# Kernel optimization log

Measured on AMD Instinct MI355X. Metric: run time of the kernel, lower is better.

Reference implementation:

```python
import jax, jax.numpy as jnp
import numpy as np

N = 500000   # num_nodes
B = 512      # batch_size
D = 128      # node_dim
G = 128      # global_dim
MC = 64      # max_cubes
M = 24       # max_moves_per_cube
H = 128      # MLP hidden
NEG = -1000000000.0


def setup_inputs() -> dict:
    key = jax.random.key(0)
    ks = jax.random.split(key, 8)
    node_features = jax.random.normal(ks[0], (N, D), jnp.float32)
    global_features = jax.random.normal(ks[1], (B, G), jnp.float32)
    cube_mask = jax.random.randint(ks[2], (N,), 0, 2) == 1
    batch = jnp.sort(jax.random.randint(ks[3], (N,), 0, B))
    move_mask = jax.random.randint(ks[4], (B, MC, M), 0, 2) == 1
    W1 = jax.random.normal(ks[5], (D + G, H), jnp.float32) * 0.05
    b1 = jnp.zeros((H,), jnp.float32)
    W2 = jax.random.normal(ks[6], (H, M), jnp.float32) * 0.05
    b2 = jnp.zeros((M,), jnp.float32)
    return {"node_features": node_features, "global_features": global_features,
            "W1": W1, "b1": b1, "W2": W2, "b2": b2,
            "cube_mask": cube_mask, "batch": batch, "move_mask": move_mask}


def reference(node_features, global_features, W1, b1, W2, b2, cube_mask, batch, move_mask):
    bsz = global_features.shape[0]
    max_cubes, moves = move_mask.shape[1], move_mask.shape[2]
    batch = batch.astype(jnp.int32)

    # gather global features per node, concat, small MLP (scores computed for all
    # nodes; only cube-node rows are ever scattered, matching the original math)
    combined = jnp.concatenate([node_features, global_features[batch]], axis=-1)  # [N, D+G]
    h = jax.nn.relu(combined @ W1 + b1)                                           # [N, H]
    scores = h @ W2 + b2                                                          # [N, M]

    # per-batch cumulative cube count (batch is sorted): cube_idx_in_batch
    mask_i = cube_mask.astype(jnp.int32)
    cum = jnp.cumsum(mask_i)                                   # inclusive prefix count of cubes
    counts = jax.ops.segment_sum(mask_i, batch, num_segments=bsz)
    offsets = jnp.concatenate([jnp.zeros((1,), jnp.int32),
                               jnp.cumsum(counts)[:-1].astype(jnp.int32)])
    cube_idx = cum - 1 - offsets[batch]                        # index of cube within its graph

    valid = cube_mask & (cube_idx < max_cubes)
    ib = jnp.where(valid, batch, bsz)      # out-of-range rows -> dropped
    ic = jnp.where(valid, cube_idx, 0)

    logits = jnp.full((bsz, max_cubes, moves), NEG, dtype=scores.dtype)
    logits = logits.at[ib, ic].set(scores, mode="drop")        # unique (ib, ic) per valid node

    logits_flat = logits.reshape(bsz, -1)
    logits_flat = jnp.where(move_mask.reshape(bsz, -1), logits_flat, NEG)
    return logits_flat
```

## Files before the change

### kernel.cpp

```cpp
#include <hip/hip_runtime.h>

typedef short bf16x8 __attribute__((ext_vector_type(8)));
typedef float f32x4 __attribute__((ext_vector_type(4)));

#define NEGV -1000000000.0f

__device__ __forceinline__ unsigned short f2bf(float f) {
    unsigned int u = __float_as_uint(f);
    u += 0x7FFFu + ((u >> 16) & 1u);
    return (unsigned short)(u >> 16);
}

__global__ void prep_kernel(const float* __restrict__ W1, const float* __restrict__ W2,
                            const int* __restrict__ batch, int N, int B,
                            int* __restrict__ batch_start,
                            unsigned short* __restrict__ w1t, unsigned short* __restrict__ w2t) {
    int idx = blockIdx.x * 256 + threadIdx.x;
    if (idx < N) {
        int bcur = batch[idx];
        if (idx == 0) {
            for (int bb = 0; bb <= bcur; ++bb) batch_start[bb] = 0;
        } else {
            int bprev = batch[idx - 1];
            for (int bb = bprev + 1; bb <= bcur; ++bb) batch_start[bb] = idx;
        }
        if (idx == N - 1) {
            for (int bb = bcur + 1; bb <= B; ++bb) batch_start[bb] = N;
        }
    }
    if (idx < 128 * 256) {
        int col = idx >> 8, k = idx & 255;
        w1t[col * 256 + k] = f2bf(W1[k * 128 + col]);
    }
    if (idx < 32 * 128) {
        int col = idx >> 7, k = idx & 127;
        w2t[col * 128 + k] = (col < 24) ? f2bf(W2[k * 24 + col]) : (unsigned short)0;
    }
}

__global__ void __launch_bounds__(256, 2)
fused_kernel(const float* __restrict__ nf, const float* __restrict__ gf,
             const unsigned short* __restrict__ w1t, const unsigned short* __restrict__ w2t,
             const float* __restrict__ b1, const float* __restrict__ b2,
             const int* __restrict__ cube_mask, const int* __restrict__ batch_start,
             const int* __restrict__ move_mask, float* __restrict__ out) {
    __shared__ __align__(16) unsigned short ldsA[64][72];
    __shared__ __align__(16) unsigned short ldsB[128][72];
    __shared__ __align__(16) unsigned short ldsH[64][136];
    __shared__ __align__(16) unsigned short ldsW2[32][136];
    __shared__ int lds_node[64];
    __shared__ int wt[4];

    int t = threadIdx.x;
    int blk = blockIdx.x;
    int lane = t & 63, w = t >> 6;

    if (t < 64) lds_node[t] = -1;
    {
        int col = t >> 3;
        int k0 = (t & 7) * 16;
        const unsigned short* src = w2t + col * 128 + k0;
        *(bf16x8*)&ldsW2[col][k0]     = *(const bf16x8*)(src);
        *(bf16x8*)&ldsW2[col][k0 + 8] = *(const bf16x8*)(src + 8);
    }
    int segs = batch_start[blk], sege = batch_start[blk + 1];
    __syncthreads();

    int found = 0;
    for (int pos = segs; pos < sege && found < 64; pos += 256) {
        int i = pos + t;
        int m = (i < sege) ? cube_mask[i] : 0;
        unsigned long long bal = __ballot(m != 0);
        int below = __popcll(bal & ((1ULL << lane) - 1ULL));
        if (lane == 0) wt[w] = __popcll(bal);
        __syncthreads();
        int waveOfs = 0, total = 0;
#pragma unroll
        for (int j = 0; j < 4; ++j) { int c = wt[j]; if (j < w) waveOfs += c; total += c; }
        int rank = found + waveOfs + below;
        if (m && rank < 64) lds_node[rank] = i;
        found += total;
        __syncthreads();
    }
    __syncthreads();

    int wm = w >> 1, wn = w & 1;
    f32x4 acc[2][4];
#pragma unroll
    for (int i = 0; i < 2; ++i)
#pragma unroll
        for (int j = 0; j < 4; ++j) acc[i][j] = (f32x4){0.f, 0.f, 0.f, 0.f};

    int r = t >> 2;
    int q = t & 3;
    int n = lds_node[r];
    int nrow = (n >= 0) ? n : 0;

    float4 fA[4];
    bf16x8 fB[4];
    int bcol = t >> 1;
    int bh0 = (t & 1) * 32;

#define LOAD_A(c) do { \
        const float* srcA = ((c) < 2) ? nf + (size_t)nrow * 128 + (c) * 64 + q * 16 \
                                      : gf + (size_t)blk * 128 + ((c) - 2) * 64 + q * 16; \
        fA[0] = *(const float4*)(srcA);      fA[1] = *(const float4*)(srcA + 4); \
        fA[2] = *(const float4*)(srcA + 8);  fA[3] = *(const float4*)(srcA + 12); \
    } while (0)
#define LOAD_B(c) do { \
        const unsigned short* srcB = w1t + bcol * 256 + (c) * 64 + bh0; \
        fB[0] = *(const bf16x8*)(srcB);      fB[1] = *(const bf16x8*)(srcB + 8); \
        fB[2] = *(const bf16x8*)(srcB + 16); fB[3] = *(const bf16x8*)(srcB + 24); \
    } while (0)

    LOAD_A(0); LOAD_B(0);
#pragma unroll
    for (int c = 0; c < 4; ++c) {
        {
            unsigned short tmp[16];
#pragma unroll
            for (int i = 0; i < 4; ++i) {
                tmp[i * 4 + 0] = f2bf(fA[i].x); tmp[i * 4 + 1] = f2bf(fA[i].y);
                tmp[i * 4 + 2] = f2bf(fA[i].z); tmp[i * 4 + 3] = f2bf(fA[i].w);
            }
            *(bf16x8*)&ldsA[r][q * 16]     = *(bf16x8*)&tmp[0];
            *(bf16x8*)&ldsA[r][q * 16 + 8] = *(bf16x8*)&tmp[8];
            *(bf16x8*)&ldsB[bcol][bh0]      = fB[0];
            *(bf16x8*)&ldsB[bcol][bh0 + 8]  = fB[1];
            *(bf16x8*)&ldsB[bcol][bh0 + 16] = fB[2];
            *(bf16x8*)&ldsB[bcol][bh0 + 24] = fB[3];
        }
        __syncthreads();
        if (c < 3) { LOAD_A(c + 1); LOAD_B(c + 1); }
#pragma unroll
        for (int ks = 0; ks < 2; ++ks) {
            int ko = ks * 32 + (lane >> 4) * 8;
            bf16x8 af[2], bfr[4];
#pragma unroll
            for (int mt = 0; mt < 2; ++mt)
                af[mt] = *(const bf16x8*)&ldsA[wm * 32 + mt * 16 + (lane & 15)][ko];
#pragma unroll
            for (int nt = 0; nt < 4; ++nt)
                bfr[nt] = *(const bf16x8*)&ldsB[wn * 64 + nt * 16 + (lane & 15)][ko];
#pragma unroll
            for (int mt = 0; mt < 2; ++mt)
#pragma unroll
                for (int nt = 0; nt < 4; ++nt)
                    acc[mt][nt] = __builtin_amdgcn_mfma_f32_16x16x32_bf16(
                        af[mt], bfr[nt], acc[mt][nt], 0, 0, 0);
        }
        __syncthreads();
    }
#undef LOAD_A
#undef LOAD_B

#pragma unroll
    for (int nt = 0; nt < 4; ++nt) {
        int col = wn * 64 + nt * 16 + (lane & 15);
        float bias = b1[col];
#pragma unroll
        for (int mt = 0; mt < 2; ++mt) {
            int row0 = wm * 32 + mt * 16 + (lane >> 4) * 4;
#pragma unroll
            for (int rr = 0; rr < 4; ++rr) {
                float v = acc[mt][nt][rr] + bias;
                v = v > 0.f ? v : 0.f;
                ldsH[row0 + rr][col] = f2bf(v);
            }
        }
    }
    __syncthreads();

    f32x4 acc2[2];
    acc2[0] = (f32x4){0.f, 0.f, 0.f, 0.f};
    acc2[1] = (f32x4){0.f, 0.f, 0.f, 0.f};
#pragma unroll
    for (int ks = 0; ks < 4; ++ks) {
        int ko = ks * 32 + (lane >> 4) * 8;
        bf16x8 a2 = *(const bf16x8*)&ldsH[w * 16 + (lane & 15)][ko];
#pragma unroll
        for (int ct = 0; ct < 2; ++ct) {
            bf16x8 bw = *(const bf16x8*)&ldsW2[ct * 16 + (lane & 15)][ko];
            acc2[ct] = __builtin_amdgcn_mfma_f32_16x16x32_bf16(a2, bw, acc2[ct], 0, 0, 0);
        }
    }

#pragma unroll
    for (int ct = 0; ct < 2; ++ct) {
        int m = ct * 16 + (lane & 15);
        if (m >= 24) continue;
        float bias = b2[m];
#pragma unroll
        for (int rr = 0; rr < 4; ++rr) {
            int row = w * 16 + (lane >> 4) * 4 + rr;
            int slot = blk * 64 + row;
            size_t oidx = (size_t)slot * 24 + m;
            float v = acc2[ct][rr] + bias;
            bool keep = (lds_node[row] >= 0) && (move_mask[oidx] != 0);
            out[oidx] = keep ? v : NEGV;
        }
    }
}

extern "C" void kernel_launch(void* const* d_in, const int* in_sizes, int n_in,
                              void* d_out, int out_size, void* d_ws, size_t ws_size,
                              hipStream_t stream) {
    const float* nf = (const float*)d_in[0];
    const float* gf = (const float*)d_in[1];
    const float* W1 = (const float*)d_in[2];
    const float* b1 = (const float*)d_in[3];
    const float* W2 = (const float*)d_in[4];
    const float* b2 = (const float*)d_in[5];
    const int* cube_mask = (const int*)d_in[6];
    const int* batch     = (const int*)d_in[7];
    const int* move_mask = (const int*)d_in[8];
    float* out = (float*)d_out;

    int N = in_sizes[6];
    int B = in_sizes[1] / 128;

    char* ws = (char*)d_ws;
    int* batch_start = (int*)(ws);
    unsigned short* w1t = (unsigned short*)(ws + 4096);
    unsigned short* w2t = (unsigned short*)(ws + 69632);

    int NB = (N + 255) / 256;
    prep_kernel<<<NB, 256, 0, stream>>>(W1, W2, batch, N, B, batch_start, w1t, w2t);
    fused_kernel<<<B, 256, 0, stream>>>(nf, gf, w1t, w2t, b1, b2,
                                        cube_mask, batch_start, move_mask, out);
    (void)n_in; (void)out_size; (void)ws_size;
}
```

Measured before the change: 20.15 us.

## Hoist weight, bias and mask loads early, prefetch node rows, alias LDS

The fused kernel now issues the first W1 tile, the biases and the move_mask values before the cube-compaction scan, so their latency hides behind the scan. Both node-feature chunks are loaded right after compaction instead of chunk by chunk. The H buffer is aliased onto the A/B staging LDS, and launch bounds go from 2 to 3 blocks per SM to allow more occupancy. The cost is higher register pressure from the extra prefetched values, which may cause spills under the tighter launch bound.

Result: faster. 17.86 us, median of 3 (-11.4%).

```diff
diff --git a/kernel.cpp b/kernel.cpp
--- a/kernel.cpp
+++ b/kernel.cpp
@@ -38,24 +38,28 @@
     }
 }
 
-__global__ void __launch_bounds__(256, 2)
+__global__ void __launch_bounds__(256, 3)
 fused_kernel(const float* __restrict__ nf, const float* __restrict__ gf,
              const unsigned short* __restrict__ w1t, const unsigned short* __restrict__ w2t,
              const float* __restrict__ b1, const float* __restrict__ b2,
              const int* __restrict__ cube_mask, const int* __restrict__ batch_start,
              const int* __restrict__ move_mask, float* __restrict__ out) {
-    __shared__ __align__(16) unsigned short ldsA[64][72];
-    __shared__ __align__(16) unsigned short ldsB[128][72];
-    __shared__ __align__(16) unsigned short ldsH[64][136];
+    __shared__ __align__(16) char smemAB[(64 * 72 + 128 * 72) * 2];
     __shared__ __align__(16) unsigned short ldsW2[32][136];
     __shared__ int lds_node[64];
     __shared__ int wt[4];
+    unsigned short (*ldsA)[72]  = (unsigned short (*)[72])smemAB;
+    unsigned short (*ldsB)[72]  = (unsigned short (*)[72])(smemAB + 64 * 72 * 2);
+    unsigned short (*ldsH)[136] = (unsigned short (*)[136])smemAB;
 
     int t = threadIdx.x;
     int blk = blockIdx.x;
     int lane = t & 63, w = t >> 6;
 
+    int segs = batch_start[blk], sege = batch_start[blk + 1];
+
     if (t < 64) lds_node[t] = -1;
+
     {
         int col = t >> 3;
         int k0 = (t & 7) * 16;
@@ -63,7 +67,35 @@
         *(bf16x8*)&ldsW2[col][k0]     = *(const bf16x8*)(src);
         *(bf16x8*)&ldsW2[col][k0 + 8] = *(const bf16x8*)(src + 8);
     }
-    int segs = batch_start[blk], sege = batch_start[blk + 1];
+    int bcol = t >> 1, bh0 = (t & 1) * 32;
+    bf16x8 fB[4];
+    {
+        const unsigned short* srcB = w1t + bcol * 256 + bh0;
+        fB[0] = *(const bf16x8*)(srcB);      fB[1] = *(const bf16x8*)(srcB + 8);
+        fB[2] = *(const bf16x8*)(srcB + 16); fB[3] = *(const bf16x8*)(srcB + 24);
+    }
+    int wm = w >> 1, wn = w & 1;
+    float b1v[4];
+#pragma unroll
+    for (int nt = 0; nt < 4; ++nt) b1v[nt] = b1[wn * 64 + nt * 16 + (lane & 15)];
+    float b2v[2];
+    int mmv[8];
+#pragma unroll
+    for (int ct = 0; ct < 2; ++ct) {
+        int m = ct * 16 + (lane & 15);
+        if (m < 24) {
+            b2v[ct] = b2[m];
+#pragma unroll
+            for (int rr = 0; rr < 4; ++rr) {
+                int row = w * 16 + (lane >> 4) * 4 + rr;
+                mmv[ct * 4 + rr] = move_mask[(size_t)(blk * 64 + row) * 24 + m];
+            }
+        } else {
+            b2v[ct] = 0.f;
+#pragma unroll
+            for (int rr = 0; rr < 4; ++rr) mmv[ct * 4 + rr] = 0;
+        }
+    }
     __syncthreads();
 
     int found = 0;
@@ -82,47 +114,40 @@
         found += total;
         __syncthreads();
     }
-    __syncthreads();
-
-    int wm = w >> 1, wn = w & 1;
-    f32x4 acc[2][4];
-#pragma unroll
-    for (int i = 0; i < 2; ++i)
-#pragma unroll
-        for (int j = 0; j < 4; ++j) acc[i][j] = (f32x4){0.f, 0.f, 0.f, 0.f};
 
     int r = t >> 2;
     int q = t & 3;
     int n = lds_node[r];
     int nrow = (n >= 0) ? n : 0;
 
+    const float* srcN = nf + (size_t)nrow * 128 + q * 16;
+    float4 fN[8];
+#pragma unroll
+    for (int i = 0; i < 4; ++i) {
+        fN[i]     = *(const float4*)(srcN + i * 4);
+        fN[4 + i] = *(const float4*)(srcN + 64 + i * 4);
+    }
+
+    f32x4 acc[2][4];
+#pragma unroll
+    for (int i = 0; i < 2; ++i)
+#pragma unroll
+        for (int j = 0; j < 4; ++j) acc[i][j] = (f32x4){0.f, 0.f, 0.f, 0.f};
+
     float4 fA[4];
-    bf16x8 fB[4];
-    int bcol = t >> 1;
-    int bh0 = (t & 1) * 32;
-
-#define LOAD_A(c) do { \
-        const float* srcA = ((c) < 2) ? nf + (size_t)nrow * 128 + (c) * 64 + q * 16 \
-                                      : gf + (size_t)blk * 128 + ((c) - 2) * 64 + q * 16; \
-        fA[0] = *(const float4*)(srcA);      fA[1] = *(const float4*)(srcA + 4); \
-        fA[2] = *(const float4*)(srcA + 8);  fA[3] = *(const float4*)(srcA + 12); \
-    } while (0)
-#define LOAD_B(c) do { \
-        const unsigned short* srcB = w1t + bcol * 256 + (c) * 64 + bh0; \
-        fB[0] = *(const bf16x8*)(srcB);      fB[1] = *(const bf16x8*)(srcB + 8); \
-        fB[2] = *(const bf16x8*)(srcB + 16); fB[3] = *(const bf16x8*)(srcB + 24); \
-    } while (0)
-
-    LOAD_A(0); LOAD_B(0);
+
 #pragma unroll
     for (int c = 0; c < 4; ++c) {
         {
+            float4 s0 = (c == 0) ? fN[0] : (c == 1) ? fN[4] : fA[0];
+            float4 s1 = (c == 0) ? fN[1] : (c == 1) ? fN[5] : fA[1];
+            float4 s2 = (c == 0) ? fN[2] : (c == 1) ? fN[6] : fA[2];
+            float4 s3 = (c == 0) ? fN[3] : (c == 1) ? fN[7] : fA[3];
             unsigned short tmp[16];
-#pragma unroll
-            for (int i = 0; i < 4; ++i) {
-                tmp[i * 4 + 0] = f2bf(fA[i].x); tmp[i * 4 + 1] = f2bf(fA[i].y);
-                tmp[i * 4 + 2] = f2bf(fA[i].z); tmp[i * 4 + 3] = f2bf(fA[i].w);
-            }
+            tmp[0]  = f2bf(s0.x); tmp[1]  = f2bf(s0.y); tmp[2]  = f2bf(s0.z); tmp[3]  = f2bf(s0.w);
+            tmp[4]  = f2bf(s1.x); tmp[5]  = f2bf(s1.y); tmp[6]  = f2bf(s1.z); tmp[7]  = f2bf(s1.w);
+            tmp[8]  = f2bf(s2.x); tmp[9]  = f2bf(s2.y); tmp[10] = f2bf(s2.z); tmp[11] = f2bf(s2.w);
+            tmp[12] = f2bf(s3.x); tmp[13] = f2bf(s3.y); tmp[14] = f2bf(s3.z); tmp[15] = f2bf(s3.w);
             *(bf16x8*)&ldsA[r][q * 16]     = *(bf16x8*)&tmp[0];
             *(bf16x8*)&ldsA[r][q * 16 + 8] = *(bf16x8*)&tmp[8];
             *(bf16x8*)&ldsB[bcol][bh0]      = fB[0];
@@ -131,7 +156,16 @@
             *(bf16x8*)&ldsB[bcol][bh0 + 24] = fB[3];
         }
         __syncthreads();
-        if (c < 3) { LOAD_A(c + 1); LOAD_B(c + 1); }
+        if (c < 3) {
+            const unsigned short* srcB = w1t + bcol * 256 + (c + 1) * 64 + bh0;
+            fB[0] = *(const bf16x8*)(srcB);      fB[1] = *(const bf16x8*)(srcB + 8);
+            fB[2] = *(const bf16x8*)(srcB + 16); fB[3] = *(const bf16x8*)(srcB + 24);
+        }
+        if (c == 1 || c == 2) {
+            const float* srcG = gf + (size_t)blk * 128 + (c - 1) * 64 + q * 16;
+            fA[0] = *(const float4*)(srcG);     fA[1] = *(const float4*)(srcG + 4);
+            fA[2] = *(const float4*)(srcG + 8); fA[3] = *(const float4*)(srcG + 12);
+        }
 #pragma unroll
         for (int ks = 0; ks < 2; ++ks) {
             int ko = ks * 32 + (lane >> 4) * 8;
@@ -151,13 +185,11 @@
         }
         __syncthreads();
     }
-#undef LOAD_A
-#undef LOAD_B
 
 #pragma unroll
     for (int nt = 0; nt < 4; ++nt) {
         int col = wn * 64 + nt * 16 + (lane & 15);
-        float bias = b1[col];
+        float bias = b1v[nt];
 #pragma unroll
         for (int mt = 0; mt < 2; ++mt) {
             int row0 = wm * 32 + mt * 16 + (lane >> 4) * 4;
@@ -189,14 +221,12 @@
     for (int ct = 0; ct < 2; ++ct) {
         int m = ct * 16 + (lane & 15);
         if (m >= 24) continue;
-        float bias = b2[m];
 #pragma unroll
         for (int rr = 0; rr < 4; ++rr) {
             int row = w * 16 + (lane >> 4) * 4 + rr;
-            int slot = blk * 64 + row;
-            size_t oidx = (size_t)slot * 24 + m;
-            float v = acc2[ct][rr] + bias;
-            bool keep = (lds_node[row] >= 0) && (move_mask[oidx] != 0);
+            size_t oidx = (size_t)(blk * 64 + row) * 24 + m;
+            float v = acc2[ct][rr] + b2v[ct];
+            bool keep = (lds_node[row] >= 0) && (mmv[ct * 4 + rr] != 0);
             out[oidx] = keep ? v : NEGV;
         }
     }
```
